# Kernel optimization log

Measured on AMD Instinct MI355X. Metric: run time of the kernel, lower is better.

The kernel has to match this reference:

```python
import jax, jax.numpy as jnp
import numpy as np

EMBED_DIM = 1024
HEADS = 16
HEAD_DIM = EMBED_DIM // HEADS
N, SEQ = 2, 2048


def setup_inputs() -> dict:
    key = jax.random.key(0)
    ks = jax.random.split(key, 9)
    s = 1.0 / np.sqrt(HEAD_DIM)
    inp = {
        "values": jax.random.normal(ks[0], (N, SEQ, EMBED_DIM), jnp.float32),
        "keys": jax.random.normal(ks[1], (N, SEQ, EMBED_DIM), jnp.float32),
        "query": jax.random.normal(ks[2], (N, SEQ, EMBED_DIM), jnp.float32),
        "mask": jax.random.randint(ks[3], (N, 1, SEQ, SEQ), 0, 2, jnp.int32),
        # per-head projection weights (torch Linear: y = x @ W.T)
        "Wv": jax.random.normal(ks[4], (HEAD_DIM, HEAD_DIM), jnp.float32) * s,
        "Wk": jax.random.normal(ks[5], (HEAD_DIM, HEAD_DIM), jnp.float32) * s,
        "Wq": jax.random.normal(ks[6], (HEAD_DIM, HEAD_DIM), jnp.float32) * s,
        "Wo": jax.random.normal(ks[7], (EMBED_DIM, EMBED_DIM), jnp.float32) * (1.0 / np.sqrt(EMBED_DIM)),
        "bo": jax.random.normal(ks[8], (EMBED_DIM,), jnp.float32) * 0.01,
    }
    return inp


def reference(values, keys, query, mask, Wv, Wk, Wq, Wo, bo):
    n, q_len = query.shape[0], query.shape[1]
    v_len, k_len = values.shape[1], keys.shape[1]
    # reshape to [N, len, H, D]
    v = values.reshape(n, v_len, HEADS, HEAD_DIM)
    k = keys.reshape(n, k_len, HEADS, HEAD_DIM)
    q = query.reshape(n, q_len, HEADS, HEAD_DIM)
    # per-head linear projections (shared weight across heads), torch: x @ W.T
    v = jnp.einsum("nlhd,ed->nlhe", v, Wv)
    k = jnp.einsum("nlhd,ed->nlhe", k, Wk)
    q = jnp.einsum("nlhd,ed->nlhe", q, Wq)
    # energy: [N, H, Q, K]
    energy = jnp.einsum("nqhd,nkhd->nhqk", q, k)
    energy = jnp.where(mask == 0, jnp.float32(-1e20), energy)
    # NOTE: original scales by sqrt(embed_dim), not sqrt(head_dim)
    attention = jax.nn.softmax(energy / jnp.sqrt(jnp.float32(EMBED_DIM)), axis=3)
    out = jnp.einsum("nhql,nlhd->nqhd", attention, v).reshape(n, q_len, EMBED_DIM)
    out = out @ Wo.T + bo  # fc_out; dropout is identity in eval mode
    return out
```

## Files before the change

kernel.cpp:

```cpp
#include <hip/hip_runtime.h>
#include <hip/hip_bf16.h>

#define NB 2
#define SEQ 2048
#define HEADS 16
#define HD 64
#define ED 1024

typedef __bf16 bf16x8 __attribute__((ext_vector_type(8)));
typedef float f32x4 __attribute__((ext_vector_type(4)));
typedef unsigned short u16x8 __attribute__((ext_vector_type(8)));
typedef unsigned short u16x4 __attribute__((ext_vector_type(4)));

__device__ __forceinline__ unsigned short f2bf(float f) {
    unsigned u = __builtin_bit_cast(unsigned, f);
    u += 0x7fffu + ((u >> 16) & 1u);
    return (unsigned short)(u >> 16);
}

__device__ __forceinline__ bf16x8 cvt8(const float* __restrict__ p) {
    const float4* p4 = (const float4*)p;
    float4 a = p4[0], b = p4[1];
    u16x8 u;
    u[0] = f2bf(a.x); u[1] = f2bf(a.y); u[2] = f2bf(a.z); u[3] = f2bf(a.w);
    u[4] = f2bf(b.x); u[5] = f2bf(b.y); u[6] = f2bf(b.z); u[7] = f2bf(b.w);
    return __builtin_bit_cast(bf16x8, u);
}

__device__ __forceinline__ bf16x8 ldfrag(const void* p) {
    uint4 v = *(const uint4*)p;
    return __builtin_bit_cast(bf16x8, v);
}

__device__ __forceinline__ f32x4 mfma16(bf16x8 a, bf16x8 b, f32x4 c) {
    return __builtin_amdgcn_mfma_f32_16x16x32_bf16(a, b, c, 0, 0, 0);
}

__device__ __forceinline__ unsigned packbf(float lo, float hi) {
    unsigned a = __builtin_bit_cast(unsigned, hi) + 0x8000u;
    unsigned b = __builtin_bit_cast(unsigned, lo) + 0x8000u;
    return __builtin_amdgcn_perm(a, b, 0x07060302u);
}

#define GLOAD_LDS(gp, lp) \
    __builtin_amdgcn_global_load_lds( \
        (const __attribute__((address_space(1))) unsigned int*)(gp), \
        (__attribute__((address_space(3))) unsigned int*)(lp), 16, 0, 0)

#define QSCALE 0.04508422f

__global__ __launch_bounds__(256) void mask_bits_kernel(
    const int* __restrict__ mask, unsigned long long* __restrict__ bits)
{
    size_t i = (size_t)blockIdx.x * 256 + threadIdx.x;
    int m = mask[i];
    unsigned long long b = __ballot(m != 0);
    if ((threadIdx.x & 63) == 0) bits[i >> 6] = b;
}

__global__ __launch_bounds__(256) void wo_cvt_kernel(
    const float* __restrict__ Wo, unsigned short* __restrict__ Wob)
{
    size_t i = ((size_t)blockIdx.x * 256 + threadIdx.x) * 4;
    float4 v = *(const float4*)(Wo + i);
    u16x4 u;
    u[0] = f2bf(v.x); u[1] = f2bf(v.y); u[2] = f2bf(v.z); u[3] = f2bf(v.w);
    *(u16x4*)(Wob + i) = u;
}

__global__ __launch_bounds__(256) void proj_kernel(
    const float* __restrict__ qin, const float* __restrict__ kin, const float* __restrict__ vin,
    const float* __restrict__ Wq, const float* __restrict__ Wk, const float* __restrict__ Wv,
    unsigned short* __restrict__ Qb, unsigned short* __restrict__ Kb,
    unsigned short* __restrict__ Vt)
{
    __shared__ __align__(16) char tile[64 * 144];

    int t3  = blockIdx.x >> 10;
    int rem = blockIdx.x & 1023;
    int h   = rem >> 6;
    int rt  = rem & 63;
    int wave = threadIdx.x >> 6, lane = threadIdx.x & 63;
    int quad = lane >> 4, l16 = lane & 15;

    const float* in = (t3 == 0) ? qin : ((t3 == 1) ? kin : vin);
    const float* W  = (t3 == 0) ? Wq  : ((t3 == 1) ? Wk  : Wv);

    int r0 = rt * 64 + wave * 16;

    bf16x8 bf0[4], bf1[4];
#pragma unroll
    for (int sl = 0; sl < 4; ++sl) {
        const float* wrow = W + (sl * 16 + l16) * 64;
        bf0[sl] = cvt8(wrow + quad * 8);
        bf1[sl] = cvt8(wrow + 32 + quad * 8);
    }
    const float* xrow = in + (size_t)(r0 + l16) * ED + h * 64;
    bf16x8 af0 = cvt8(xrow + quad * 8);
    bf16x8 af1 = cvt8(xrow + 32 + quad * 8);

    f32x4 acc[4];
#pragma unroll
    for (int sl = 0; sl < 4; ++sl) {
        f32x4 c = {0.f, 0.f, 0.f, 0.f};
        c = mfma16(af0, bf0[sl], c);
        c = mfma16(af1, bf1[sl], c);
        acc[sl] = c;
    }
    float sc = (t3 == 0) ? QSCALE : 1.0f;

    size_t nh = (size_t)((r0 >> 11) * HEADS + h);
    int rl = lane >> 3, cl = lane & 7;

    if (t3 != 2) {
#pragma unroll
        for (int r = 0; r < 4; ++r) {
            int srow = wave * 16 + quad * 4 + r;
#pragma unroll
            for (int sl = 0; sl < 4; ++sl)
                *(unsigned short*)(tile + srow * 144 + (sl * 16 + l16) * 2) =
                    f2bf(acc[sl][r] * sc);
        }
        unsigned short* dst = (t3 == 0) ? Qb : Kb;
        int s0 = (r0 & 2047);
#pragma unroll
        for (int g = 0; g < 2; ++g) {
            int lrow = wave * 16 + g * 8 + rl;
            uint4 v = *(const uint4*)(tile + lrow * 144 + cl * 16);
            *(uint4*)(dst + (nh * SEQ + (s0 & ~15) + g * 8 + rl) * HD + cl * 8) = v;
        }
    } else {
#pragma unroll
        for (int r = 0; r < 4; ++r) {
            int srow = wave * 16 + quad * 4 + r;
#pragma unroll
            for (int sl = 0; sl < 4; ++sl)
                *(unsigned short*)(tile + (sl * 16 + l16) * 144 + srow * 2) =
                    f2bf(acc[sl][r]);
        }
        __syncthreads();
        int s_tile = rt & 31;
#pragma unroll
        for (int g = 0; g < 2; ++g) {
            int erow = wave * 16 + g * 8 + rl;
            uint4 v = *(const uint4*)(tile + erow * 144 + cl * 16);
            *(uint4*)(Vt + ((nh * 32 + s_tile) * 64 + erow) * 64 + cl * 8) = v;
        }
    }
}

template <int SPLIT>
__global__ __launch_bounds__(256, 4) void attn_kernel(
    const unsigned short* __restrict__ Qb, const unsigned short* __restrict__ Kb,
    const unsigned short* __restrict__ Vt2, const unsigned long long* __restrict__ mb,
    unsigned short* __restrict__ Ab, float* __restrict__ Of, float* __restrict__ Ls)
{
    __shared__ __align__(16) char smem[24576 + 4 * 2304];

    int tid = threadIdx.x;
    int wave = tid >> 6, lane = tid & 63;
    int quad = lane >> 4, l16 = lane & 15;

    int b   = blockIdx.x;
    int xcd = b & 7;
    int j   = b >> 3;
    int nh, qb, half;
    if (SPLIT) { nh = xcd * 4 + (j >> 5); int r = j & 31; qb = r >> 1; half = r & 1; }
    else       { nh = xcd * 4 + (j >> 4); qb = j & 15; half = 0; }
    int n = nh >> 4, h = nh & 15;
    int q0 = qb * 128 + wave * 32;

    size_t headoff = (size_t)nh * SEQ * HD;
    bf16x8 qf[2][2];
#pragma unroll
    for (int t = 0; t < 2; ++t) {
        const unsigned short* qrow = Qb + headoff + (size_t)(q0 + t * 16 + l16) * HD;
        qf[t][0] = ldfrag(qrow + quad * 8);
        qf[t][1] = ldfrag(qrow + 32 + quad * 8);
    }

    int srow = lane >> 3, sslot = lane & 7;
    int stoff = srow * 128 + (((sslot - srow) & 7) * 16);

    int rotA = ((quad + l16) & 7) * 16;
    int aK0 = l16 * 128 + rotA;
    int aV  = 16384 + l16 * 128 + rotA;
    int aVx = aV ^ 64;
    char* pbase = smem + 24576 + wave * 2304;
    char* pw = pbase + l16 * 144 + quad * 8;
    char* pr = pbase + l16 * 144 + quad * 16;

    const unsigned short* gK = Kb + headoff;
    const unsigned short* gV = Vt2 + (size_t)nh * (32 * 4096);
    const unsigned long long* mbase = mb + (size_t)n * (SEQ * SEQ / 64)
                                         + (size_t)(q0 + l16) * (SEQ / 64);

    u16x8 ou;
#pragma unroll
    for (int jj = 0; jj < 8; ++jj) ou[jj] = 0x3F80;
    bf16x8 ones = __builtin_bit_cast(bf16x8, ou);

    f32x4 o[2][4] = {{{0,0,0,0},{0,0,0,0},{0,0,0,0},{0,0,0,0}},
                     {{0,0,0,0},{0,0,0,0},{0,0,0,0},{0,0,0,0}}};
    f32x4 lacc[2] = {{0,0,0,0},{0,0,0,0}};
    int qsh = quad * 4;

    int kb0   = SPLIT ? half * (SEQ / 2) : 0;
    int kbend = SPLIT ? kb0 + (SEQ / 2) : SEQ;

    {
        const char* sK = (const char*)(gK + (size_t)kb0 * 64) + stoff;
        const char* sV = (const char*)(gV + (size_t)(kb0 >> 6) * 4096) + stoff;
#pragma unroll
        for (int i2 = 0; i2 < 2; ++i2) {
            int c = wave * 2 + i2;
            GLOAD_LDS(sK + c * 1024, smem + c * 1024);
            GLOAD_LDS(sV + c * 1024, smem + 16384 + c * 1024);
        }
    }

    int par = 0;
    for (int kb = kb0; kb < kbend; kb += 64) {
        int kbn = (kb + 64) & (SEQ - 1);
        __syncthreads();
        {
            const char* sK = (const char*)(gK + (size_t)kbn * 64) + stoff;
            char* dK = smem + (par ^ 1) * 8192;
#pragma unroll
            for (int i2 = 0; i2 < 2; ++i2) {
                int c = wave * 2 + i2;
                GLOAD_LDS(sK + c * 1024, dK + c * 1024);
            }
        }
        unsigned long long m64[2];
#pragma unroll
        for (int t = 0; t < 2; ++t)
            m64[t] = mbase[(size_t)(t * 16) * (SEQ / 64) + (kb >> 6)] >> qsh;

        const char* kbuf = smem + par * 8192;
        bf16x8 kf[4][2];
#pragma unroll
        for (int kt = 0; kt < 4; ++kt) {
            kf[kt][0] = ldfrag(kbuf + aK0 + kt * 2048);
            kf[kt][1] = ldfrag(kbuf + (aK0 ^ 64) + kt * 2048);
        }
#pragma unroll
        for (int t = 0; t < 2; ++t) {
            f32x4 c[4];
#pragma unroll
            for (int kt = 0; kt < 4; ++kt) {
                f32x4 cc = {0.f, 0.f, 0.f, 0.f};
                cc = mfma16(kf[kt][0], qf[t][0], cc);
                cc = mfma16(kf[kt][1], qf[t][1], cc);
                c[kt] = cc;
            }
            unsigned mlo = (unsigned)m64[t];
            unsigned mhi = (unsigned)(m64[t] >> 32);
#pragma unroll
            for (int kt = 0; kt < 4; ++kt) {
                unsigned mw = (kt & 2) ? mhi : mlo;
                int bs = (kt & 1) ? 16 : 0;
                float p0 = ((mw >> (bs + 0)) & 1u) ? __builtin_exp2f(c[kt][0]) : 0.f;
                float p1 = ((mw >> (bs + 1)) & 1u) ? __builtin_exp2f(c[kt][1]) : 0.f;
                float p2 = ((mw >> (bs + 2)) & 1u) ? __builtin_exp2f(c[kt][2]) : 0.f;
                float p3 = ((mw >> (bs + 3)) & 1u) ? __builtin_exp2f(c[kt][3]) : 0.f;
                uint2 dw = { packbf(p0, p1), packbf(p2, p3) };
                *(uint2*)(pw + kt * 32) = dw;
            }
            bf16x8 pb0 = ldfrag(pr);
            bf16x8 pb1 = ldfrag(pr + 64);
            lacc[t] = mfma16(ones, pb0, lacc[t]);
            lacc[t] = mfma16(ones, pb1, lacc[t]);
#pragma unroll
            for (int sl = 0; sl < 4; ++sl) {
                o[t][sl] = mfma16(ldfrag(smem + aV  + sl * 2048), pb0, o[t][sl]);
                o[t][sl] = mfma16(ldfrag(smem + aVx + sl * 2048), pb1, o[t][sl]);
            }
        }
        __syncthreads();
        {
            const char* sV = (const char*)(gV + (size_t)(kbn >> 6) * 4096) + stoff;
#pragma unroll
            for (int i2 = 0; i2 < 2; ++i2) {
                int c = wave * 2 + i2;
                GLOAD_LDS(sV + c * 1024, smem + 16384 + c * 1024);
            }
        }
        par ^= 1;
    }

#pragma unroll
    for (int t = 0; t < 2; ++t) {
        float s = lacc[t][0];
        int q = q0 + t * 16 + l16;
        if (SPLIT) {
            size_t qg = (size_t)nh * SEQ + q;
            if (quad == 0) Ls[(size_t)half * 65536 + qg] = s;
            float* op = Of + ((size_t)half * 65536 + qg) * 64 + qsh;
#pragma unroll
            for (int sl = 0; sl < 4; ++sl) {
                float4 v = { o[t][sl][0], o[t][sl][1], o[t][sl][2], o[t][sl][3] };
                *(float4*)(op + sl * 16) = v;
            }
        } else {
            float rinv = 1.0f / s;
            unsigned short* op = Ab + (((size_t)(n * SEQ + q)) * HEADS + h) * HD + qsh;
#pragma unroll
            for (int sl = 0; sl < 4; ++sl) {
                u16x4 u;
                u[0] = f2bf(o[t][sl][0] * rinv);
                u[1] = f2bf(o[t][sl][1] * rinv);
                u[2] = f2bf(o[t][sl][2] * rinv);
                u[3] = f2bf(o[t][sl][3] * rinv);
                *(u16x4*)(op + sl * 16) = u;
            }
        }
    }
}

__global__ __launch_bounds__(256) void combine_kernel(
    const float* __restrict__ Of, const float* __restrict__ Ls,
    unsigned short* __restrict__ Ab)
{
    int idx = blockIdx.x * 256 + threadIdx.x;
    int q  = idx >> 4;
    int d0 = (idx & 15) * 4;
    const float4 o0 = *(const float4*)(Of + (size_t)q * 64 + d0);
    const float4 o1 = *(const float4*)(Of + 4194304 + (size_t)q * 64 + d0);
    float rl = 1.0f / (Ls[q] + Ls[65536 + q]);
    int n = q >> 15, h = (q >> 11) & 15, s = q & 2047;
    size_t ab = (((size_t)(n * SEQ + s)) * HEADS + h) * HD + d0;
    u16x4 u;
    u[0] = f2bf((o0.x + o1.x) * rl);
    u[1] = f2bf((o0.y + o1.y) * rl);
    u[2] = f2bf((o0.z + o1.z) * rl);
    u[3] = f2bf((o0.w + o1.w) * rl);
    *(u16x4*)(Ab + ab) = u;
}

__global__ __launch_bounds__(256) void out_gemm_kernel(
    const unsigned short* __restrict__ Ab, const unsigned short* __restrict__ Wob,
    const float* __restrict__ bo, float* __restrict__ out)
{
    __shared__ __align__(16) char lds[32768];

    int wave = threadIdx.x >> 6, lane = threadIdx.x & 63;
    int quad = lane >> 4, l16 = lane & 15;
    int rt = blockIdx.x >> 3, ct = blockIdx.x & 7;
    int wr = wave >> 1, wc = wave & 1;

    int srow = lane >> 3, sslot = lane & 7;
    int stoff = srow * 2048 + (((sslot - srow) & 7) * 16);
    const char* gA = (const char*)Ab  + (size_t)rt * 128 * 2048 + stoff;
    const char* gB = (const char*)Wob + (size_t)ct * 128 * 2048 + stoff;

    int aA[4], aB[4];
#pragma unroll
    for (int i = 0; i < 4; ++i) {
        int rowA = wr * 64 + i * 16 + l16;
        aA[i] = rowA * 128 + (((quad + rowA) & 7) * 16);
        int rowB = wc * 64 + i * 16 + l16;
        aB[i] = 16384 + rowB * 128 + (((quad + rowB) & 7) * 16);
    }

    f32x4 acc[4][4] = {};
    for (int f = 0; f < ED; f += 64) {
        __syncthreads();
#pragma unroll
        for (int i = 0; i < 4; ++i) {
            int c = wave * 4 + i;
            GLOAD_LDS(gA + (size_t)c * 16384 + f * 2, lds + c * 1024);
            GLOAD_LDS(gB + (size_t)c * 16384 + f * 2, lds + 16384 + c * 1024);
        }
        __syncthreads();
#pragma unroll
        for (int kk = 0; kk < 2; ++kk) {
            int x = kk * 64;
            bf16x8 af[4], bfr[4];
#pragma unroll
            for (int i = 0; i < 4; ++i)  af[i]  = ldfrag(lds + (aA[i] ^ x));
#pragma unroll
            for (int sl = 0; sl < 4; ++sl) bfr[sl] = ldfrag(lds + (aB[sl] ^ x));
#pragma unroll
            for (int i = 0; i < 4; ++i)
#pragma unroll
                for (int sl = 0; sl < 4; ++sl)
                    acc[i][sl] = mfma16(af[i], bfr[sl], acc[i][sl]);
        }
    }

    float bv[4];
#pragma unroll
    for (int sl = 0; sl < 4; ++sl)
        bv[sl] = bo[ct * 128 + wc * 64 + sl * 16 + l16];
#pragma unroll
    for (int i = 0; i < 4; ++i)
#pragma unroll
        for (int r = 0; r < 4; ++r) {
            int row = rt * 128 + wr * 64 + i * 16 + quad * 4 + r;
#pragma unroll
            for (int sl = 0; sl < 4; ++sl) {
                int e = ct * 128 + wc * 64 + sl * 16 + l16;
                out[(size_t)row * ED + e] = acc[i][sl][r] + bv[sl];
            }
        }
}

extern "C" void kernel_launch(void* const* d_in, const int* in_sizes, int n_in,
                              void* d_out, int out_size, void* d_ws, size_t ws_size,
                              hipStream_t stream)
{
    const float* values = (const float*)d_in[0];
    const float* keys   = (const float*)d_in[1];
    const float* query  = (const float*)d_in[2];
    const int*   mask   = (const int*)d_in[3];
    const float* Wv     = (const float*)d_in[4];
    const float* Wk     = (const float*)d_in[5];
    const float* Wq     = (const float*)d_in[6];
    const float* Wo     = (const float*)d_in[7];
    const float* bo     = (const float*)d_in[8];
    float* out = (float*)d_out;

    char* w = (char*)d_ws;
    unsigned short* Qb  = (unsigned short*)(w);
    unsigned short* Kb  = (unsigned short*)(w +  8388608);
    unsigned short* Vt  = (unsigned short*)(w + 16777216);
    unsigned short* Ab  = (unsigned short*)(w + 25165824);
    unsigned long long* Mb = (unsigned long long*)(w + 33554432);
    unsigned short* Wob = (unsigned short*)(w + 34603008);
    float* Of = (float*)(w + 36700160);
    float* Ls = (float*)(w + 70254592);

    bool split = ws_size >= 70778880ULL;

    mask_bits_kernel<<<NB * SEQ * SEQ / 256, 256, 0, stream>>>(mask, Mb);
    wo_cvt_kernel<<<ED * ED / (256 * 4), 256, 0, stream>>>(Wo, Wob);
    proj_kernel<<<3 * HEADS * 64, 256, 0, stream>>>(query, keys, values, Wq, Wk, Wv, Qb, Kb, Vt);
    if (split) {
        attn_kernel<1><<<1024, 256, 0, stream>>>(Qb, Kb, Vt, Mb, Ab, Of, Ls);
        combine_kernel<<<4096, 256, 0, stream>>>(Of, Ls, Ab);
    } else {
        attn_kernel<0><<<512, 256, 0, stream>>>(Qb, Kb, Vt, Mb, Ab, Of, Ls);
    }
    out_gemm_kernel<<<256, 256, 0, stream>>>(Ab, Wob, bo, out);
}
```

Baseline: 252.6 us.

## Fuse split-K combine into output GEMM, store partials as bf16, double-buffer V

The mask-bit and Wo-conversion kernels become one launch. The attention kernel now double-buffers V alongside K, which removes the second barrier per key block, and it uses a swizzled P staging layout to cut LDS bank conflicts. The split-K partial outputs are written as bf16 instead of fp32, and the separate combine kernel is removed: the output GEMM reads both halves, normalises them and writes the A tile into LDS itself. This saves a launch and cuts partial-output traffic, at the cost of bf16 precision on the partials and synchronous A-tile loads in the GEMM.

```diff
diff --git a/kernel.cpp b/kernel.cpp
--- a/kernel.cpp
+++ b/kernel.cpp
@@ -42,6 +42,14 @@
     return __builtin_amdgcn_perm(a, b, 0x07060302u);
 }
 
+__device__ __forceinline__ unsigned comb2(unsigned d0, unsigned d1, float rl) {
+    float lo = (__builtin_bit_cast(float, d0 << 16) +
+                __builtin_bit_cast(float, d1 << 16)) * rl;
+    float hi = (__builtin_bit_cast(float, d0 & 0xffff0000u) +
+                __builtin_bit_cast(float, d1 & 0xffff0000u)) * rl;
+    return packbf(lo, hi);
+}
+
 #define GLOAD_LDS(gp, lp) \
     __builtin_amdgcn_global_load_lds( \
         (const __attribute__((address_space(1))) unsigned int*)(gp), \
@@ -49,23 +57,23 @@
 
 #define QSCALE 0.04508422f
 
-__global__ __launch_bounds__(256) void mask_bits_kernel(
-    const int* __restrict__ mask, unsigned long long* __restrict__ bits)
-{
-    size_t i = (size_t)blockIdx.x * 256 + threadIdx.x;
-    int m = mask[i];
-    unsigned long long b = __ballot(m != 0);
-    if ((threadIdx.x & 63) == 0) bits[i >> 6] = b;
-}
-
-__global__ __launch_bounds__(256) void wo_cvt_kernel(
+__global__ __launch_bounds__(256) void prep_kernel(
+    const int* __restrict__ mask, unsigned long long* __restrict__ bits,
     const float* __restrict__ Wo, unsigned short* __restrict__ Wob)
 {
-    size_t i = ((size_t)blockIdx.x * 256 + threadIdx.x) * 4;
-    float4 v = *(const float4*)(Wo + i);
-    u16x4 u;
-    u[0] = f2bf(v.x); u[1] = f2bf(v.y); u[2] = f2bf(v.z); u[3] = f2bf(v.w);
-    *(u16x4*)(Wob + i) = u;
+    int bid = blockIdx.x;
+    if (bid < NB * SEQ * SEQ / 256) {
+        size_t i = (size_t)bid * 256 + threadIdx.x;
+        int m = mask[i];
+        unsigned long long b = __ballot(m != 0);
+        if ((threadIdx.x & 63) == 0) bits[i >> 6] = b;
+    } else {
+        size_t i = ((size_t)(bid - NB * SEQ * SEQ / 256) * 256 + threadIdx.x) * 4;
+        float4 v = *(const float4*)(Wo + i);
+        u16x4 u;
+        u[0] = f2bf(v.x); u[1] = f2bf(v.y); u[2] = f2bf(v.z); u[3] = f2bf(v.w);
+        *(u16x4*)(Wob + i) = u;
+    }
 }
 
 __global__ __launch_bounds__(256) void proj_kernel(
@@ -153,9 +161,10 @@
 __global__ __launch_bounds__(256, 4) void attn_kernel(
     const unsigned short* __restrict__ Qb, const unsigned short* __restrict__ Kb,
     const unsigned short* __restrict__ Vt2, const unsigned long long* __restrict__ mb,
-    unsigned short* __restrict__ Ab, float* __restrict__ Of, float* __restrict__ Ls)
+    unsigned short* __restrict__ Ab, unsigned short* __restrict__ Of,
+    float* __restrict__ Ls)
 {
-    __shared__ __align__(16) char smem[24576 + 4 * 2304];
+    __shared__ __align__(16) char smem[40960];
 
     int tid = threadIdx.x;
     int wave = tid >> 6, lane = tid & 63;
@@ -183,12 +192,13 @@
     int stoff = srow * 128 + (((sslot - srow) & 7) * 16);
 
     int rotA = ((quad + l16) & 7) * 16;
-    int aK0 = l16 * 128 + rotA;
-    int aV  = 16384 + l16 * 128 + rotA;
-    int aVx = aV ^ 64;
-    char* pbase = smem + 24576 + wave * 2304;
-    char* pw = pbase + l16 * 144 + quad * 8;
-    char* pr = pbase + l16 * 144 + quad * 16;
+    int aK  = l16 * 128 + rotA;
+    int aV  = l16 * 128 + rotA;
+
+    int r8 = l16 & 7, q1 = quad & 1, q2 = quad >> 1;
+    char* pP = smem + 32768 + wave * 2048;
+    int pwoff = l16 * 128 + q1 * 8 + ((q2 ^ (r8 & 1)) * 16) + ((r8 & 6) * 16);
+    int proff = l16 * 128 + ((quad ^ r8) * 16);
 
     const unsigned short* gK = Kb + headoff;
     const unsigned short* gV = Vt2 + (size_t)nh * (32 * 4096);
@@ -224,12 +234,14 @@
         int kbn = (kb + 64) & (SEQ - 1);
         __syncthreads();
         {
-            const char* sK = (const char*)(gK + (size_t)kbn * 64) + stoff;
-            char* dK = smem + (par ^ 1) * 8192;
+            const char* nK = (const char*)(gK + (size_t)kbn * 64) + stoff;
+            const char* nV = (const char*)(gV + (size_t)(kbn >> 6) * 4096) + stoff;
+            int pb8 = (par ^ 1) * 8192;
 #pragma unroll
             for (int i2 = 0; i2 < 2; ++i2) {
                 int c = wave * 2 + i2;
-                GLOAD_LDS(sK + c * 1024, dK + c * 1024);
+                GLOAD_LDS(nK + c * 1024, smem + pb8 + c * 1024);
+                GLOAD_LDS(nV + c * 1024, smem + 16384 + pb8 + c * 1024);
             }
         }
         unsigned long long m64[2];
@@ -238,11 +250,12 @@
             m64[t] = mbase[(size_t)(t * 16) * (SEQ / 64) + (kb >> 6)] >> qsh;
 
         const char* kbuf = smem + par * 8192;
+        const char* vbuf = smem + 16384 + par * 8192;
         bf16x8 kf[4][2];
 #pragma unroll
         for (int kt = 0; kt < 4; ++kt) {
-            kf[kt][0] = ldfrag(kbuf + aK0 + kt * 2048);
-            kf[kt][1] = ldfrag(kbuf + (aK0 ^ 64) + kt * 2048);
+            kf[kt][0] = ldfrag(kbuf + (aK + kt * 2048));
+            kf[kt][1] = ldfrag(kbuf + ((aK ^ 64) + kt * 2048));
         }
 #pragma unroll
         for (int t = 0; t < 2; ++t) {
@@ -265,25 +278,16 @@
                 float p2 = ((mw >> (bs + 2)) & 1u) ? __builtin_exp2f(c[kt][2]) : 0.f;
                 float p3 = ((mw >> (bs + 3)) & 1u) ? __builtin_exp2f(c[kt][3]) : 0.f;
                 uint2 dw = { packbf(p0, p1), packbf(p2, p3) };
-                *(uint2*)(pw + kt * 32) = dw;
-            }
-            bf16x8 pb0 = ldfrag(pr);
-            bf16x8 pb1 = ldfrag(pr + 64);
+                *(uint2*)(pP + (pwoff ^ (kt * 32))) = dw;
+            }
+            bf16x8 pb0 = ldfrag(pP + proff);
+            bf16x8 pb1 = ldfrag(pP + (proff ^ 64));
             lacc[t] = mfma16(ones, pb0, lacc[t]);
             lacc[t] = mfma16(ones, pb1, lacc[t]);
 #pragma unroll
             for (int sl = 0; sl < 4; ++sl) {
-                o[t][sl] = mfma16(ldfrag(smem + aV  + sl * 2048), pb0, o[t][sl]);
-                o[t][sl] = mfma16(ldfrag(smem + aVx + sl * 2048), pb1, o[t][sl]);
-            }
-        }
-        __syncthreads();
-        {
-            const char* sV = (const char*)(gV + (size_t)(kbn >> 6) * 4096) + stoff;
-#pragma unroll
-            for (int i2 = 0; i2 < 2; ++i2) {
-                int c = wave * 2 + i2;
-                GLOAD_LDS(sV + c * 1024, smem + 16384 + c * 1024);
+                o[t][sl] = mfma16(ldfrag(vbuf + (aV + sl * 2048)), pb0, o[t][sl]);
+                o[t][sl] = mfma16(ldfrag(vbuf + ((aV ^ 64) + sl * 2048)), pb1, o[t][sl]);
             }
         }
         par ^= 1;
@@ -296,11 +300,12 @@
         if (SPLIT) {
             size_t qg = (size_t)nh * SEQ + q;
             if (quad == 0) Ls[(size_t)half * 65536 + qg] = s;
-            float* op = Of + ((size_t)half * 65536 + qg) * 64 + qsh;
+            unsigned short* op = Of + ((size_t)half * 32 * SEQ + qg) * 64 + qsh;
 #pragma unroll
             for (int sl = 0; sl < 4; ++sl) {
-                float4 v = { o[t][sl][0], o[t][sl][1], o[t][sl][2], o[t][sl][3] };
-                *(float4*)(op + sl * 16) = v;
+                uint2 dw = { packbf(o[t][sl][0], o[t][sl][1]),
+                             packbf(o[t][sl][2], o[t][sl][3]) };
+                *(uint2*)(op + sl * 16) = dw;
             }
         } else {
             float rinv = 1.0f / s;
@@ -318,33 +323,16 @@
     }
 }
 
-__global__ __launch_bounds__(256) void combine_kernel(
-    const float* __restrict__ Of, const float* __restrict__ Ls,
-    unsigned short* __restrict__ Ab)
-{
-    int idx = blockIdx.x * 256 + threadIdx.x;
-    int q  = idx >> 4;
-    int d0 = (idx & 15) * 4;
-    const float4 o0 = *(const float4*)(Of + (size_t)q * 64 + d0);
-    const float4 o1 = *(const float4*)(Of + 4194304 + (size_t)q * 64 + d0);
-    float rl = 1.0f / (Ls[q] + Ls[65536 + q]);
-    int n = q >> 15, h = (q >> 11) & 15, s = q & 2047;
-    size_t ab = (((size_t)(n * SEQ + s)) * HEADS + h) * HD + d0;
-    u16x4 u;
-    u[0] = f2bf((o0.x + o1.x) * rl);
-    u[1] = f2bf((o0.y + o1.y) * rl);
-    u[2] = f2bf((o0.z + o1.z) * rl);
-    u[3] = f2bf((o0.w + o1.w) * rl);
-    *(u16x4*)(Ab + ab) = u;
-}
-
+template <int FUSED>
 __global__ __launch_bounds__(256) void out_gemm_kernel(
-    const unsigned short* __restrict__ Ab, const unsigned short* __restrict__ Wob,
+    const unsigned short* __restrict__ Ab, const unsigned short* __restrict__ Of,
+    const float* __restrict__ Ls, const unsigned short* __restrict__ Wob,
     const float* __restrict__ bo, float* __restrict__ out)
 {
     __shared__ __align__(16) char lds[32768];
 
-    int wave = threadIdx.x >> 6, lane = threadIdx.x & 63;
+    int tid = threadIdx.x;
+    int wave = tid >> 6, lane = tid & 63;
     int quad = lane >> 4, l16 = lane & 15;
     int rt = blockIdx.x >> 3, ct = blockIdx.x & 7;
     int wr = wave >> 1, wc = wave & 1;
@@ -353,6 +341,10 @@
     int stoff = srow * 2048 + (((sslot - srow) & 7) * 16);
     const char* gA = (const char*)Ab  + (size_t)rt * 128 * 2048 + stoff;
     const char* gB = (const char*)Wob + (size_t)ct * 128 * 2048 + stoff;
+
+    int nbase = (rt >> 4) * 16;
+    int sb    = (rt & 15) * 128;
+    int r0l = tid >> 3, slot = tid & 7;
 
     int aA[4], aB[4];
 #pragma unroll
@@ -366,11 +358,36 @@
     f32x4 acc[4][4] = {};
     for (int f = 0; f < ED; f += 64) {
         __syncthreads();
-#pragma unroll
-        for (int i = 0; i < 4; ++i) {
-            int c = wave * 4 + i;
-            GLOAD_LDS(gA + (size_t)c * 16384 + f * 2, lds + c * 1024);
-            GLOAD_LDS(gB + (size_t)c * 16384 + f * 2, lds + 16384 + c * 1024);
+        if (FUSED) {
+            int nh2 = nbase + (f >> 6);
+            const unsigned short* of0 = Of + ((size_t)nh2 * SEQ + sb) * 64;
+            const unsigned short* of1 = of0 + (size_t)32 * SEQ * 64;
+            const float* ls0 = Ls + (size_t)nh2 * SEQ + sb;
+#pragma unroll
+            for (int k = 0; k < 4; ++k) {
+                int row = r0l + k * 32;
+                uint4 a0 = *(const uint4*)(of0 + (size_t)row * 64 + slot * 8);
+                uint4 a1 = *(const uint4*)(of1 + (size_t)row * 64 + slot * 8);
+                float rl = 1.0f / (ls0[row] + ls0[65536 + row]);
+                uint4 w;
+                w.x = comb2(a0.x, a1.x, rl);
+                w.y = comb2(a0.y, a1.y, rl);
+                w.z = comb2(a0.z, a1.z, rl);
+                w.w = comb2(a0.w, a1.w, rl);
+                *(uint4*)(lds + row * 128 + (((slot + row) & 7) * 16)) = w;
+            }
+#pragma unroll
+            for (int i = 0; i < 4; ++i) {
+                int c = wave * 4 + i;
+                GLOAD_LDS(gB + (size_t)c * 16384 + f * 2, lds + 16384 + c * 1024);
+            }
+        } else {
+#pragma unroll
+            for (int i = 0; i < 4; ++i) {
+                int c = wave * 4 + i;
+                GLOAD_LDS(gA + (size_t)c * 16384 + f * 2, lds + c * 1024);
+                GLOAD_LDS(gB + (size_t)c * 16384 + f * 2, lds + 16384 + c * 1024);
+            }
         }
         __syncthreads();
 #pragma unroll
@@ -428,19 +445,18 @@
     unsigned short* Ab  = (unsigned short*)(w + 25165824);
     unsigned long long* Mb = (unsigned long long*)(w + 33554432);
     unsigned short* Wob = (unsigned short*)(w + 34603008);
-    float* Of = (float*)(w + 36700160);
-    float* Ls = (float*)(w + 70254592);
-
-    bool split = ws_size >= 70778880ULL;
-
-    mask_bits_kernel<<<NB * SEQ * SEQ / 256, 256, 0, stream>>>(mask, Mb);
-    wo_cvt_kernel<<<ED * ED / (256 * 4), 256, 0, stream>>>(Wo, Wob);
+    unsigned short* Of  = (unsigned short*)(w + 36700160);
+    float* Ls = (float*)(w + 53477376);
+
+    bool split = ws_size >= 54001664ULL;
+
+    prep_kernel<<<NB * SEQ * SEQ / 256 + ED * ED / 1024, 256, 0, stream>>>(mask, Mb, Wo, Wob);
     proj_kernel<<<3 * HEADS * 64, 256, 0, stream>>>(query, keys, values, Wq, Wk, Wv, Qb, Kb, Vt);
     if (split) {
         attn_kernel<1><<<1024, 256, 0, stream>>>(Qb, Kb, Vt, Mb, Ab, Of, Ls);
-        combine_kernel<<<4096, 256, 0, stream>>>(Of, Ls, Ab);
+        out_gemm_kernel<1><<<256, 256, 0, stream>>>(Ab, Of, Ls, Wob, bo, out);
     } else {
         attn_kernel<0><<<512, 256, 0, stream>>>(Qb, Kb, Vt, Mb, Ab, Of, Ls);
-    }
-    out_gemm_kernel<<<256, 256, 0, stream>>>(Ab, Wob, bo, out);
-}
+        out_gemm_kernel<0><<<256, 256, 0, stream>>>(Ab, Of, Ls, Wob, bo, out);
+    }
+}
```

Result: slower. 277.4 us (+9.8%).
